# Kernel tuning notes

Measured on AMD Instinct MI355X. Metric: run time of the kernel, lower is better.

## Reference

```python
import jax, jax.numpy as jnp
import numpy as np

L = 2          # n_layer
H = 8          # n_head
DM = 512       # d_model
DFF = 2048     # d_ff
DH = DM // H   # head dim (query_dimensions)
M = DH         # Favor n_dims random features
B, S = 1, 2048
EPS = 1e-6     # causal linear attention eps
LN_EPS = 1e-5  # torch LayerNorm default


def setup_inputs() -> dict:
    key = jax.random.key(0)
    ks = jax.random.split(key, 12)
    sc = 0.02
    d = {}
    d['x'] = jax.random.normal(ks[0], (B, S, DM), dtype=jnp.float32)
    for i, (n, shape) in enumerate([('Wq', (L, DM, DM)), ('Wk', (L, DM, DM)),
                                    ('Wv', (L, DM, DM)), ('Wo', (L, DM, DM)),
                                    ('W1', (L, DM, DFF)), ('W2', (L, DFF, DM))]):
        d[n] = jax.random.normal(ks[i + 1], shape, dtype=jnp.float32) * sc
    d['bq'] = jnp.zeros((L, DM), jnp.float32)
    d['bk'] = jnp.zeros((L, DM), jnp.float32)
    d['bv'] = jnp.zeros((L, DM), jnp.float32)
    d['bo'] = jnp.zeros((L, DM), jnp.float32)
    d['b1'] = jnp.zeros((L, DFF), jnp.float32)
    d['b2'] = jnp.zeros((L, DM), jnp.float32)
    d['g1'] = jnp.ones((L, DM), jnp.float32)
    d['be1'] = jnp.zeros((L, DM), jnp.float32)
    d['g2'] = jnp.ones((L, DM), jnp.float32)
    d['be2'] = jnp.zeros((L, DM), jnp.float32)
    # FAVOR+ random projection matrix per layer: [Dh, M]
    d['omega'] = jax.random.normal(ks[7], (L, DH, M), dtype=jnp.float32)
    return d


def _favor(x, omega):
    # x: [B,S,H,Dh]; softmax_temp = 1/sqrt(Dh) applied as x * sqrt(temp)
    xs = x * (DH ** -0.25)
    nrm = jnp.sum(xs * xs, axis=-1, keepdims=True)       # [B,S,H,1]
    u = jnp.einsum('bshd,dm->bshm', xs, omega)           # [B,S,H,M]
    return jnp.exp(u - 0.5 * nrm) * (M ** -0.5)


def _ln(x, g, b):
    mu = jnp.mean(x, -1, keepdims=True)
    var = jnp.mean((x - mu) ** 2, -1, keepdims=True)
    return (x - mu) * jax.lax.rsqrt(var + LN_EPS) * g + b


def _forward(x, Wq, bq, Wk, bk, Wv, bv, Wo, bo, omega,
             W1, b1, W2, b2, g1, be1, g2, be2):
    out = x
    for l in range(L):
        q = (out @ Wq[l] + bq[l]).reshape(B, S, H, DH)
        k = (out @ Wk[l] + bk[l]).reshape(B, S, H, DH)
        v = (out @ Wv[l] + bv[l]).reshape(B, S, H, DH)
        pq = _favor(q, omega[l])
        pk = _favor(k, omega[l])
        # causal linear attention: running sums of phi(k) v^T and phi(k)
        kv = jnp.cumsum(jnp.einsum('bshm,bshd->bshmd', pk, v), axis=1)  # [B,S,H,M,Dh]
        num = jnp.einsum('bshm,bshmd->bshd', pq, kv)
        den = jnp.einsum('bshm,bshm->bsh', pq, jnp.cumsum(pk, axis=1)) + EPS
        a = (num / den[..., None]).reshape(B, S, DM)
        # post-norm encoder layer (fast-transformers TransformerEncoderLayer)
        out = out + (a @ Wo[l] + bo[l])
        out = _ln(out, g1[l], be1[l])
        y = jax.nn.relu(out @ W1[l] + b1[l]) @ W2[l] + b2[l]
        out = _ln(out + y, g2[l], be2[l])
    return out


def reference(x, Wq, bq, Wk, bk, Wv, bv, Wo, bo, omega,
              W1, b1, W2, b2, g1, be1, g2, be2):
    return _forward(x, Wq, bq, Wk, bk, Wv, bv, Wo, bo, omega,
                    W1, b1, W2, b2, g1, be1, g2, be2)
```

## Files before the change

### kernel.cpp

```cpp
#include <hip/hip_runtime.h>
#include <hip/hip_bf16.h>

#define S_  2048
#define DM_ 512
#define H_  8
#define DH_ 64
#define MF_ 64
#define DFF_ 2048
#define L_  2
#define CT_ 64
#define NC_ (S_ / CT_)
#define EPS_ 1e-6f
#define LN_EPS_ 1e-5f

#define LSW_   3145728
#define W1OFF_ 1048576
#define W2OFF_ 2097152
#define WOOFF_ 786432

typedef unsigned short ushortT;
typedef unsigned int u32;
typedef float f4 __attribute__((ext_vector_type(4)));
typedef short s8 __attribute__((ext_vector_type(8)));
typedef u32 u32x2 __attribute__((ext_vector_type(2)));

__device__ __forceinline__ ushortT f2b(float f) {
  union { float f; unsigned u; } v; v.f = f;
  unsigned r = v.u + 0x7fffu + ((v.u >> 16) & 1u);
  return (ushortT)(r >> 16);
}
__device__ __forceinline__ float bu2f(ushortT h) {
  union { unsigned u; float f; } v; v.u = ((unsigned)h) << 16; return v.f;
}
__device__ __forceinline__ u32 pk2(float a, float b) {
  return (u32)f2b(a) | ((u32)f2b(b) << 16);
}

__global__ __launch_bounds__(256) void tcast_all(
    const float* __restrict__ x,
    const float* __restrict__ Wq, const float* __restrict__ Wk,
    const float* __restrict__ Wv, const float* __restrict__ Wo,
    const float* __restrict__ W1, const float* __restrict__ W2,
    const float* __restrict__ omg,
    float* __restrict__ cur, ushortT* __restrict__ curb,
    ushortT* __restrict__ wb, ushortT* __restrict__ omgTb) {
  const int bid = blockIdx.x;
  const int t = threadIdx.x;
  if (bid >= 6152) {
    const int i = (bid - 6152) * 256 + t;
    float v = x[i];
    cur[i] = v;
    curb[i] = f2b(v);
    return;
  }
  __shared__ ushortT tile[32][33];
  const float* src; ushortT* dst; int K, N, bx, by;
  if (bid < 2048) {
    const int z = bid >> 8, widx = z & 3, lay = z >> 2;
    const float* s4[4] = {Wq, Wk, Wv, Wo};
    src = s4[widx] + (size_t)lay * DM_ * DM_;
    dst = wb + (size_t)lay * LSW_ + (size_t)widx * DM_ * DM_;
    K = DM_; N = DM_; bx = bid & 15; by = (bid >> 4) & 15;
  } else if (bid < 4096) {
    const int r = bid - 2048;
    const int lay = r >> 10;
    src = W1 + (size_t)lay * DM_ * DFF_;
    dst = wb + (size_t)lay * LSW_ + W1OFF_;
    K = DM_; N = DFF_; bx = r & 63; by = (r >> 6) & 15;
  } else if (bid < 6144) {
    const int r = bid - 4096;
    const int lay = r >> 10;
    src = W2 + (size_t)lay * DFF_ * DM_;
    dst = wb + (size_t)lay * LSW_ + W2OFF_;
    K = DFF_; N = DM_; bx = r & 15; by = (r >> 4) & 63;
  } else {
    const int r = bid - 6144;
    const int lay = r >> 2;
    src = omg + (size_t)lay * DH_ * MF_;
    dst = omgTb + (size_t)lay * DH_ * MF_;
    K = DH_; N = MF_; bx = r & 1; by = (r >> 1) & 1;
  }
  const int cc = t & 31, r0 = t >> 5;
  const int n0 = bx * 32, k0 = by * 32;
#pragma unroll
  for (int i = 0; i < 4; ++i) {
    int r = r0 + 8 * i;
    tile[r][cc] = f2b(src[(size_t)(k0 + r) * N + n0 + cc]);
  }
  __syncthreads();
#pragma unroll
  for (int i = 0; i < 4; ++i) {
    int r = r0 + 8 * i;
    dst[(size_t)(n0 + r) * K + k0 + cc] = tile[cc][r];
  }
}

template<bool RELU, bool HAS_RES, bool OUT_BF16>
__global__ __launch_bounds__(256) void mgemm(
    const ushortT* __restrict__ A, const ushortT* __restrict__ Wt,
    const float* __restrict__ bq_, const float* __restrict__ bk_,
    const float* __restrict__ bv_, const float* __restrict__ Res,
    float* __restrict__ Cf, ushortT* __restrict__ Cb, int K, int N) {
  __shared__ ushortT sA[2][2048];
  __shared__ ushortT sB[2][2048];
  const int t = threadIdx.x;
  const int w = t >> 6, l = t & 63;
  const int wm = w >> 1, wn = w & 1;
  const int n0 = blockIdx.x * 64, m0 = blockIdx.y * 64;
  const int z = blockIdx.z;
  const ushortT* Wz = Wt + (size_t)z * K * N;
  const float* bias = (z == 0) ? bq_ : (z == 1 ? bk_ : bv_);

  const int rs = w * 16 + (l >> 2);
  const int qs = (l & 3) ^ ((rs >> 1) & 3);
  const ushortT* gA = A  + (size_t)(m0 + rs) * K + qs * 8;
  const ushortT* gB = Wz + (size_t)(n0 + rs) * K + qs * 8;

  const int Ra = wm * 32 + (l & 15);
  const int Rb = wn * 32 + (l & 15);
  const int qq = l >> 4;
  const int aoff = (Ra * 4 + (qq ^ ((Ra >> 1) & 3))) * 8;
  const int boff = (Rb * 4 + (qq ^ ((Rb >> 1) & 3))) * 8;

  f4 acc[2][2];
#pragma unroll
  for (int i = 0; i < 2; ++i)
#pragma unroll
    for (int j = 0; j < 2; ++j) acc[i][j] = (f4){0.f, 0.f, 0.f, 0.f};

  auto stage = [&](int buf, int ko) {
    __builtin_amdgcn_global_load_lds(
        (const __attribute__((address_space(1))) void*)(gA + ko),
        (__attribute__((address_space(3))) void*)(&sA[buf][w * 512]), 16, 0, 0);
    __builtin_amdgcn_global_load_lds(
        (const __attribute__((address_space(1))) void*)(gB + ko),
        (__attribute__((address_space(3))) void*)(&sB[buf][w * 512]), 16, 0, 0);
  };

  stage(0, 0);
  const int nk = K >> 5;
  for (int ks = 0; ks < nk; ++ks) {
    __syncthreads();
    if (ks + 1 < nk) stage((ks + 1) & 1, (ks + 1) * 32);
    const ushortT* pa = sA[ks & 1];
    const ushortT* pb = sB[ks & 1];
    s8 a0 = *(const s8*)(pa + aoff);
    s8 a1 = *(const s8*)(pa + aoff + 512);
    s8 b0 = *(const s8*)(pb + boff);
    s8 b1 = *(const s8*)(pb + boff + 512);
    acc[0][0] = __builtin_amdgcn_mfma_f32_16x16x32_bf16(a0, b0, acc[0][0], 0, 0, 0);
    acc[0][1] = __builtin_amdgcn_mfma_f32_16x16x32_bf16(a0, b1, acc[0][1], 0, 0, 0);
    acc[1][0] = __builtin_amdgcn_mfma_f32_16x16x32_bf16(a1, b0, acc[1][0], 0, 0, 0);
    acc[1][1] = __builtin_amdgcn_mfma_f32_16x16x32_bf16(a1, b1, acc[1][1], 0, 0, 0);
  }

  const size_t outz = (size_t)z * S_ * N;
  const int colb = n0 + wn * 32 + (l & 15);
  const int rowb = m0 + wm * 32 + ((l >> 4) << 2);
#pragma unroll
  for (int mt = 0; mt < 2; ++mt) {
#pragma unroll
    for (int nt = 0; nt < 2; ++nt) {
      const int c = colb + nt * 16;
      const float bv = bias[c];
#pragma unroll
      for (int r = 0; r < 4; ++r) {
        const int rr = rowb + mt * 16 + r;
        float v = acc[mt][nt][r] + bv;
        if (HAS_RES) v += Res[(size_t)rr * N + c];
        if (RELU) v = fmaxf(v, 0.f);
        if (OUT_BF16) Cb[outz + (size_t)rr * N + c] = f2b(v);
        else          Cf[outz + (size_t)rr * N + c] = v;
      }
    }
  }
}

__global__ __launch_bounds__(256) void mgemm_part(
    const ushortT* __restrict__ A, const ushortT* __restrict__ Wt,
    float* __restrict__ PS, int K, int N, int KS) {
  __shared__ ushortT sA[2][2048];
  __shared__ ushortT sB[2][2048];
  const int t = threadIdx.x;
  const int w = t >> 6, l = t & 63;
  const int wm = w >> 1, wn = w & 1;
  const int n0 = blockIdx.x * 64, m0 = blockIdx.y * 64;
  const int z = blockIdx.z;

  const int rs = w * 16 + (l >> 2);
  const int qs = (l & 3) ^ ((rs >> 1) & 3);
  const ushortT* gA = A  + (size_t)(m0 + rs) * K + z * KS + qs * 8;
  const ushortT* gB = Wt + (size_t)(n0 + rs) * K + z * KS + qs * 8;

  const int Ra = wm * 32 + (l & 15);
  const int Rb = wn * 32 + (l & 15);
  const int qq = l >> 4;
  const int aoff = (Ra * 4 + (qq ^ ((Ra >> 1) & 3))) * 8;
  const int boff = (Rb * 4 + (qq ^ ((Rb >> 1) & 3))) * 8;

  f4 acc[2][2];
#pragma unroll
  for (int i = 0; i < 2; ++i)
#pragma unroll
    for (int j = 0; j < 2; ++j) acc[i][j] = (f4){0.f, 0.f, 0.f, 0.f};

  auto stage = [&](int buf, int ko) {
    __builtin_amdgcn_global_load_lds(
        (const __attribute__((address_space(1))) void*)(gA + ko),
        (__attribute__((address_space(3))) void*)(&sA[buf][w * 512]), 16, 0, 0);
    __builtin_amdgcn_global_load_lds(
        (const __attribute__((address_space(1))) void*)(gB + ko),
        (__attribute__((address_space(3))) void*)(&sB[buf][w * 512]), 16, 0, 0);
  };

  stage(0, 0);
  const int nk = KS >> 5;
  for (int ks = 0; ks < nk; ++ks) {
    __syncthreads();
    if (ks + 1 < nk) stage((ks + 1) & 1, (ks + 1) * 32);
    const ushortT* pa = sA[ks & 1];
    const ushortT* pb = sB[ks & 1];
    s8 a0 = *(const s8*)(pa + aoff);
    s8 a1 = *(const s8*)(pa + aoff + 512);
    s8 b0 = *(const s8*)(pb + boff);
    s8 b1 = *(const s8*)(pb + boff + 512);
    acc[0][0] = __builtin_amdgcn_mfma_f32_16x16x32_bf16(a0, b0, acc[0][0], 0, 0, 0);
    acc[0][1] = __builtin_amdgcn_mfma_f32_16x16x32_bf16(a0, b1, acc[0][1], 0, 0, 0);
    acc[1][0] = __builtin_amdgcn_mfma_f32_16x16x32_bf16(a1, b0, acc[1][0], 0, 0, 0);
    acc[1][1] = __builtin_amdgcn_mfma_f32_16x16x32_bf16(a1, b1, acc[1][1], 0, 0, 0);
  }

  float* out = PS + (size_t)z * S_ * N;
  const int colb = n0 + wn * 32 + (l & 15);
  const int rowb = m0 + wm * 32 + ((l >> 4) << 2);
#pragma unroll
  for (int mt = 0; mt < 2; ++mt) {
#pragma unroll
    for (int nt = 0; nt < 2; ++nt) {
      const int c = colb + nt * 16;
#pragma unroll
      for (int r = 0; r < 4; ++r)
        out[(size_t)(rowb + mt * 16 + r) * N + c] = acc[mt][nt][r];
    }
  }
}

__global__ __launch_bounds__(256) void redln(const float* __restrict__ PS, int nsplit,
                                             const float* __restrict__ bias,
                                             const float* __restrict__ res,
                                             const float* __restrict__ g,
                                             const float* __restrict__ be,
                                             float* __restrict__ outF,
                                             ushortT* __restrict__ outB) {
  const int s = blockIdx.x, t = threadIdx.x;
  float v0 = bias[t] + res[(size_t)s * DM_ + t];
  float v1 = bias[t + 256] + res[(size_t)s * DM_ + 256 + t];
  for (int z = 0; z < nsplit; ++z) {
    const float* p = PS + (size_t)z * S_ * DM_ + (size_t)s * DM_;
    v0 += p[t];
    v1 += p[256 + t];
  }
  float sum = v0 + v1, sq = v0 * v0 + v1 * v1;
  for (int off = 32; off > 0; off >>= 1) {
    sum += __shfl_down(sum, off);
    sq += __shfl_down(sq, off);
  }
  __shared__ float ssum[4], ssq[4];
  __shared__ float smean, srstd;
  const int w = t >> 6;
  if ((t & 63) == 0) { ssum[w] = sum; ssq[w] = sq; }
  __syncthreads();
  if (t == 0) {
    float S1 = ssum[0] + ssum[1] + ssum[2] + ssum[3];
    float S2 = ssq[0] + ssq[1] + ssq[2] + ssq[3];
    float mu = S1 / DM_;
    smean = mu;
    srstd = rsqrtf(S2 / DM_ - mu * mu + LN_EPS_);
  }
  __syncthreads();
  const float mu = smean, rs = srstd;
  float o0 = (v0 - mu) * rs * g[t] + be[t];
  float o1 = (v1 - mu) * rs * g[256 + t] + be[256 + t];
  outF[(size_t)s * DM_ + t] = o0;
  outF[(size_t)s * DM_ + 256 + t] = o1;
  if (outB) {
    outB[(size_t)s * DM_ + t] = f2b(o0);
    outB[(size_t)s * DM_ + 256 + t] = f2b(o1);
  }
}

__global__ __launch_bounds__(256) void favor_cs(const ushortT* __restrict__ qkv,
                                                const ushortT* __restrict__ omgT,
                                                ushortT* __restrict__ PQb,
                                                ushortT* __restrict__ PKb,
                                                float* __restrict__ KVcT,
                                                float* __restrict__ Kc) {
  const int c = blockIdx.x, h = blockIdx.y, t = threadIdx.x;
  const int w = t >> 6, l = t & 63, lr = l & 15, q = l >> 4;
  __shared__ ushortT xq[64 * 72], xk[64 * 72], vT[64 * 72], omT[64 * 72];
  __shared__ ushortT pq[64 * 72], pk[64 * 72], pkT[64 * 72];
  __shared__ float nrm[128];

  const ushortT* qg = qkv + (size_t)(c * CT_) * DM_ + h * DH_;
  const ushortT* kg = qg + (size_t)S_ * DM_;
  const ushortT* vg = kg + (size_t)S_ * DM_;

  for (int i = t; i < 512; i += 256) {
    const int s = i >> 3, seg = i & 7;
    *(s8*)&xq[s * 72 + seg * 8] = *(const s8*)(qg + (size_t)s * DM_ + seg * 8);
    *(s8*)&xk[s * 72 + seg * 8] = *(const s8*)(kg + (size_t)s * DM_ + seg * 8);
    s8 av = *(const s8*)(vg + (size_t)s * DM_ + seg * 8);
#pragma unroll
    for (int j = 0; j < 8; ++j) vT[(seg * 8 + j) * 72 + s] = (ushortT)av[j];
    *(s8*)&omT[s * 72 + seg * 8] = *(const s8*)(omgT + s * 64 + seg * 8);
  }
  __syncthreads();

  if (t < 128) {
    const ushortT* src = (t < 64) ? xq : xk;
    const int s = t & 63;
    float a = 0.f;
#pragma unroll
    for (int seg = 0; seg < 8; ++seg) {
      s8 vv = *(const s8*)(src + s * 72 + seg * 8);
#pragma unroll
      for (int j = 0; j < 8; ++j) {
        float f = bu2f((ushortT)vv[j]);
        a += f * f;
      }
    }
    nrm[t] = a;
  }
  __syncthreads();

  {
    const float gam = 0.35355339059327373f;
    const int s0 = w * 16;
    s8 aq0 = *(const s8*)&xq[(s0 + lr) * 72 + q * 8];
    s8 aq1 = *(const s8*)&xq[(s0 + lr) * 72 + 32 + q * 8];
    s8 ak0 = *(const s8*)&xk[(s0 + lr) * 72 + q * 8];
    s8 ak1 = *(const s8*)&xk[(s0 + lr) * 72 + 32 + q * 8];
#pragma unroll
    for (int mt = 0; mt < 4; ++mt) {
      s8 b0 = *(const s8*)&omT[(mt * 16 + lr) * 72 + q * 8];
      s8 b1 = *(const s8*)&omT[(mt * 16 + lr) * 72 + 32 + q * 8];
      f4 cq = (f4){0.f, 0.f, 0.f, 0.f}, ck = (f4){0.f, 0.f, 0.f, 0.f};
      cq = __builtin_amdgcn_mfma_f32_16x16x32_bf16(aq0, b0, cq, 0, 0, 0);
      cq = __builtin_amdgcn_mfma_f32_16x16x32_bf16(aq1, b1, cq, 0, 0, 0);
      ck = __builtin_amdgcn_mfma_f32_16x16x32_bf16(ak0, b0, ck, 0, 0, 0);
      ck = __builtin_amdgcn_mfma_f32_16x16x32_bf16(ak1, b1, ck, 0, 0, 0);
#pragma unroll
      for (int r = 0; r < 4; ++r) {
        const int sr = s0 + q * 4 + r, mc = mt * 16 + lr;
        float vq = expf(gam * cq[r] - 0.0625f * nrm[sr]) * 0.125f;
        float vk = expf(gam * ck[r] - 0.0625f * nrm[64 + sr]) * 0.125f;
        pq[sr * 72 + mc] = f2b(vq);
        ushortT hk = f2b(vk);
        pk[sr * 72 + mc] = hk;
        pkT[mc * 72 + sr] = hk;
      }
    }
  }
  __syncthreads();

  {
    const int d0 = w * 16;
    s8 a0 = *(const s8*)&vT[(d0 + lr) * 72 + q * 8];
    s8 a1 = *(const s8*)&vT[(d0 + lr) * 72 + 32 + q * 8];
    float* outb = KVcT + (size_t)(h * NC_ + c) * DH_ * MF_;
#pragma unroll
    for (int mt = 0; mt < 4; ++mt) {
      s8 b0 = *(const s8*)&pkT[(mt * 16 + lr) * 72 + q * 8];
      s8 b1 = *(const s8*)&pkT[(mt * 16 + lr) * 72 + 32 + q * 8];
      f4 cc = (f4){0.f, 0.f, 0.f, 0.f};
      cc = __builtin_amdgcn_mfma_f32_16x16x32_bf16(a0, b0, cc, 0, 0, 0);
      cc = __builtin_amdgcn_mfma_f32_16x16x32_bf16(a1, b1, cc, 0, 0, 0);
#pragma unroll
      for (int r = 0; r < 4; ++r)
        outb[(size_t)(d0 + q * 4 + r) * MF_ + mt * 16 + lr] = cc[r];
    }
  }
  if (t < 64) {
    float s = 0.f;
#pragma unroll
    for (int seg = 0; seg < 8; ++seg) {
      s8 vv = *(const s8*)&pkT[t * 72 + seg * 8];
#pragma unroll
      for (int j = 0; j < 8; ++j) s += bu2f((ushortT)vv[j]);
    }
    Kc[(size_t)(h * NC_ + c) * MF_ + t] = s;
  }
  for (int i = t; i < 512; i += 256) {
    const int s = i >> 3, seg = i & 7;
    *(s8*)(PQb + (size_t)(c * CT_ + s) * DM_ + h * MF_ + seg * 8) = *(const s8*)&pq[s * 72 + seg * 8];
    *(s8*)(PKb + (size_t)(c * CT_ + s) * DM_ + h * MF_ + seg * 8) = *(const s8*)&pk[s * 72 + seg * 8];
  }
}

__global__ __launch_bounds__(256) void attn_pfx(const ushortT* __restrict__ PQ,
                                                const ushortT* __restrict__ PK,
                                                const ushortT* __restrict__ V,
                                                const float* __restrict__ KVcT,
                                                const float* __restrict__ Kc,
                                                ushortT* __restrict__ Aout) {
  const int cc = blockIdx.x, h = blockIdx.y, t = threadIdx.x;
  const int w = t >> 6, l = t & 63;
  const int lr = l & 15, q = l >> 4;

  __shared__ ushortT pqs[64 * 72];
  __shared__ ushortT pks[64 * 72];
  __shared__ ushortT vts[64 * 72];
  __shared__ ushortT kvs[64 * 72];
  __shared__ ushortT tms[64 * 72];
  __shared__ float dpart[256];
  __shared__ float den[64];
  __shared__ float kcs[64];

  const int s0j = t >> 3, seg0 = t & 7;
  const int s1j = (t + 256) >> 3, seg1 = t & 7;
  float acc0[8], acc1[8];
#pragma unroll
  for (int j = 0; j < 8; ++j) { acc0[j] = 0.f; acc1[j] = 0.f; }

  const float* kvbase = KVcT + (size_t)(h * NC_) * DH_ * MF_;
  for (int cp = 0; cp < cc; ++cp) {
    const float* kr = kvbase + (size_t)cp * DH_ * MF_;
    f4 a0 = *(const f4*)(kr + s0j * MF_ + seg0 * 8);
    f4 a1 = *(const f4*)(kr + s0j * MF_ + seg0 * 8 + 4);
    f4 b0 = *(const f4*)(kr + s1j * MF_ + seg1 * 8);
    f4 b1 = *(const f4*)(kr + s1j * MF_ + seg1 * 8 + 4);
    acc0[0] += a0.x; acc0[1] += a0.y; acc0[2] += a0.z; acc0[3] += a0.w;
    acc0[4] += a1.x; acc0[5] += a1.y; acc0[6] += a1.z; acc0[7] += a1.w;
    acc1[0] += b0.x; acc1[1] += b0.y; acc1[2] += b0.z; acc1[3] += b0.w;
    acc1[4] += b1.x; acc1[5] += b1.y; acc1[6] += b1.z; acc1[7] += b1.w;
  }
  {
    u32* p0 = (u32*)&kvs[s0j * 72 + seg0 * 8];
    p0[0] = pk2(acc0[0], acc0[1]); p0[1] = pk2(acc0[2], acc0[3]);
    p0[2] = pk2(acc0[4], acc0[5]); p0[3] = pk2(acc0[6], acc0[7]);
    u32* p1 = (u32*)&kvs[s1j * 72 + seg1 * 8];
    p1[0] = pk2(acc1[0], acc1[1]); p1[1] = pk2(acc1[2], acc1[3]);
    p1[2] = pk2(acc1[4], acc1[5]); p1[3] = pk2(acc1[6], acc1[7]);
  }
  if (t < 64) {
    float s = 0.f;
    for (int cp = 0; cp < cc; ++cp) s += Kc[(size_t)(h * NC_ + cp) * MF_ + t];
    kcs[t] = s;
  }

  for (int i = t; i < 512; i += 256) {
    const int s = i >> 3, seg = i & 7;
    *(s8*)&pqs[s * 72 + seg * 8] = *(const s8*)(PQ + (size_t)(cc * CT_ + s) * DM_ + h * MF_ + seg * 8);
    *(s8*)&pks[s * 72 + seg * 8] = *(const s8*)(PK + (size_t)(cc * CT_ + s) * DM_ + h * MF_ + seg * 8);
    s8 av = *(const s8*)(V + (size_t)(cc * CT_ + s) * DM_ + h * DH_ + seg * 8);
#pragma unroll
    for (int j = 0; j < 8; ++j) vts[(seg * 8 + j) * 72 + s] = (ushortT)av[j];
  }
  __syncthreads();

  {
    const int s0 = w * 16;
    s8 a0 = *(const s8*)&pqs[(s0 + lr) * 72 + q * 8];
    s8 a1 = *(const s8*)&pqs[(s0 + lr) * 72 + 32 + q * 8];
#pragma unroll
    for (int tb = 0; tb < 4; ++tb) {
      f4 c = (f4){0.f, 0.f, 0.f, 0.f};
      if (tb <= w) {
        s8 b0 = *(const s8*)&pks[(tb * 16 + lr) * 72 + q * 8];
        s8 b1 = *(const s8*)&pks[(tb * 16 + lr) * 72 + 32 + q * 8];
        c = __builtin_amdgcn_mfma_f32_16x16x32_bf16(a0, b0, c, 0, 0, 0);
        c = __builtin_amdgcn_mfma_f32_16x16x32_bf16(a1, b1, c, 0, 0, 0);
      }
#pragma unroll
      for (int r = 0; r < 4; ++r) {
        float v = c[r];
        if (tb == w && lr > q * 4 + r) v = 0.f;
        tms[(s0 + q * 4 + r) * 72 + tb * 16 + lr] = f2b(v);
      }
    }
  }
  __syncthreads();

  {
    const int s = t >> 2, part = t & 3;
    float dp = 0.f;
    const u32* trow = (const u32*)&tms[s * 72 + part * 16];
#pragma unroll
    for (int j = 0; j < 8; ++j) {
      u32 u = trow[j];
      dp += bu2f((ushortT)(u & 0xffffu)) + bu2f((ushortT)(u >> 16));
    }
    const u32* qrow = (const u32*)&pqs[s * 72 + part * 16];
    const f4* kc4 = (const f4*)(kcs + part * 16);
#pragma unroll
    for (int j = 0; j < 4; ++j) {
      f4 b = kc4[j];
      u32 ua = qrow[2 * j], ub = qrow[2 * j + 1];
      dp += bu2f((ushortT)(ua & 0xffffu)) * b.x + bu2f((ushortT)(ua >> 16)) * b.y +
            bu2f((ushortT)(ub & 0xffffu)) * b.z + bu2f((ushortT)(ub >> 16)) * b.w;
    }
    dpart[t] = dp;
  }
  __syncthreads();
  if (t < 64)
    den[t] = dpart[4 * t] + dpart[4 * t + 1] + dpart[4 * t + 2] + dpart[4 * t + 3] + EPS_;
  __syncthreads();

  {
    const int d0 = w * 16;
    const int drow = d0 + lr;
    s8 akv0 = *(const s8*)&kvs[drow * 72 + q * 8];
    s8 akv1 = *(const s8*)&kvs[drow * 72 + 32 + q * 8];
    s8 av0  = *(const s8*)&vts[drow * 72 + q * 8];
    s8 av1  = *(const s8*)&vts[drow * 72 + 32 + q * 8];
#pragma unroll
    for (int sb = 0; sb < 4; ++sb) {
      const int srow = sb * 16 + lr;
      s8 bq0 = *(const s8*)&pqs[srow * 72 + q * 8];
      s8 bq1 = *(const s8*)&pqs[srow * 72 + 32 + q * 8];
      s8 bt0 = *(const s8*)&tms[srow * 72 + q * 8];
      s8 bt1 = *(const s8*)&tms[srow * 72 + 32 + q * 8];
      f4 c = (f4){0.f, 0.f, 0.f, 0.f};
      c = __builtin_amdgcn_mfma_f32_16x16x32_bf16(akv0, bq0, c, 0, 0, 0);
      c = __builtin_amdgcn_mfma_f32_16x16x32_bf16(akv1, bq1, c, 0, 0, 0);
      c = __builtin_amdgcn_mfma_f32_16x16x32_bf16(av0, bt0, c, 0, 0, 0);
      c = __builtin_amdgcn_mfma_f32_16x16x32_bf16(av1, bt1, c, 0, 0, 0);
      const float inv = 1.f / den[srow];
      u32x2 o;
      o.x = pk2(c[0] * inv, c[1] * inv);
      o.y = pk2(c[2] * inv, c[3] * inv);
      *(u32x2*)(Aout + (size_t)(cc * CT_ + srow) * DM_ + h * DH_ + d0 + q * 4) = o;
    }
  }
}

extern "C" void kernel_launch(void* const* d_in, const int* in_sizes, int n_in,
                              void* d_out, int out_size, void* d_ws, size_t ws_size,
                              hipStream_t stream) {
  const float* x    = (const float*)d_in[0];
  const float* Wq   = (const float*)d_in[1];
  const float* Wk   = (const float*)d_in[2];
  const float* Wv   = (const float*)d_in[3];
  const float* Wo   = (const float*)d_in[4];
  const float* W1   = (const float*)d_in[5];
  const float* W2   = (const float*)d_in[6];
  const float* bq   = (const float*)d_in[7];
  const float* bk   = (const float*)d_in[8];
  const float* bv   = (const float*)d_in[9];
  const float* bo   = (const float*)d_in[10];
  const float* b1   = (const float*)d_in[11];
  const float* b2   = (const float*)d_in[12];
  const float* g1   = (const float*)d_in[13];
  const float* be1  = (const float*)d_in[14];
  const float* g2   = (const float*)d_in[15];
  const float* be2  = (const float*)d_in[16];
  const float* omg  = (const float*)d_in[17];
  float* out = (float*)d_out;

  const size_t MB = 1048576;
  float* f    = (float*)d_ws;
  float* cur  = f;
  float* ln1  = f + 1 * MB;
  float* KVcb = f + 2 * MB;
  float* Kcb  = f + 3 * MB;
  float* PS   = f + 3 * MB + 16384;

  ushortT* u    = (ushortT*)(f + 8 * MB);
  ushortT* curb = u;
  ushortT* qkb  = u + 1 * MB;
  ushortT* pqb  = u + 4 * MB;
  ushortT* pkb  = u + 5 * MB;
  ushortT* qbb  = u + 6 * MB;
  ushortT* ln1b = u + 7 * MB;
  ushortT* ffb  = u + 8 * MB;
  ushortT* wb   = u + 12 * MB;
  ushortT* omgTb = wb + 2 * LSW_;

  tcast_all<<<10248, 256, 0, stream>>>(x, Wq, Wk, Wv, Wo, W1, W2, omg,
                                       cur, curb, wb, omgTb);

  const dim3 gQKV(DM_ / 64, S_ / 64, 3);
  const dim3 gFF1(DFF_ / 64, S_ / 64, 1);
  const dim3 gWo(DM_ / 64, S_ / 64, 2);
  const dim3 gW2(DM_ / 64, S_ / 64, 4);
  const dim3 gAttn(NC_, H_);

  for (int l = 0; l < L_; ++l) {
    const ushortT* wl = wb + (size_t)l * LSW_;
    const size_t bo512 = (size_t)l * DM_;
    const size_t boFF = (size_t)l * DFF_;

    mgemm<false, false, true><<<gQKV, 256, 0, stream>>>(
        curb, wl, bq + bo512, bk + bo512, bv + bo512, nullptr, nullptr, qkb, DM_, DM_);

    favor_cs<<<gAttn, 256, 0, stream>>>(qkb, omgTb + (size_t)l * DH_ * MF_,
                                        pqb, pkb, KVcb, Kcb);
    attn_pfx<<<gAttn, 256, 0, stream>>>(pqb, pkb, qkb + 2 * (size_t)S_ * DM_,
                                        KVcb, Kcb, qbb);

    mgemm_part<<<gWo, 256, 0, stream>>>(qbb, wl + WOOFF_, PS, DM_, DM_, 256);
    redln<<<S_, 256, 0, stream>>>(PS, 2, bo + bo512, cur, g1 + bo512, be1 + bo512, ln1, ln1b);

    mgemm<true, false, true><<<gFF1, 256, 0, stream>>>(
        ln1b, wl + W1OFF_, b1 + boFF, nullptr, nullptr, nullptr, nullptr, ffb, DM_, DFF_);

    mgemm_part<<<gW2, 256, 0, stream>>>(ffb, wl + W2OFF_, PS, DFF_, DM_, 512);
    const bool last = (l == L_ - 1);
    redln<<<S_, 256, 0, stream>>>(PS, 4, b2 + bo512, ln1, g2 + bo512, be2 + bo512,
                                  last ? out : cur, last ? nullptr : curb);
  }
}
```

Before: 264.8 us.

## Fuse QKV GEMM, FAVOR features and causal prefix attention into one kernel

Replaces the separate QKV GEMM, favor_cs and attn_pfx launches with a single attn_mega kernel per layer. Each block computes its 64-row by head slice of Q, K and V directly into shared memory, builds the feature maps, publishes its chunk KV/K sums, then spin-waits on per-chunk release/acquire flags before doing the prefix attention. This removes two launches and the global round-trips for qkv, PQ and PK. In exchange it relies on cross-block flag synchronisation, which assumes all earlier chunks' blocks make progress (256 blocks should fit co-resident). It uses only 256 blocks for the QKV GEMM, giving less parallelism than the previous 768-block grid.

```diff
diff --git a/kernel.cpp b/kernel.cpp
--- a/kernel.cpp
+++ b/kernel.cpp
@@ -43,9 +43,15 @@
     const float* __restrict__ W1, const float* __restrict__ W2,
     const float* __restrict__ omg,
     float* __restrict__ cur, ushortT* __restrict__ curb,
-    ushortT* __restrict__ wb, ushortT* __restrict__ omgTb) {
+    ushortT* __restrict__ wb, ushortT* __restrict__ omgTb,
+    u32* __restrict__ flags) {
   const int bid = blockIdx.x;
   const int t = threadIdx.x;
+  if (bid == 10248) {
+    flags[t] = 0u;
+    flags[t + 256] = 0u;
+    return;
+  }
   if (bid >= 6152) {
     const int i = (bid - 6152) * 256 + t;
     float v = x[i];
@@ -98,8 +104,7 @@
 template<bool RELU, bool HAS_RES, bool OUT_BF16>
 __global__ __launch_bounds__(256) void mgemm(
     const ushortT* __restrict__ A, const ushortT* __restrict__ Wt,
-    const float* __restrict__ bq_, const float* __restrict__ bk_,
-    const float* __restrict__ bv_, const float* __restrict__ Res,
+    const float* __restrict__ bias, const float* __restrict__ Res,
     float* __restrict__ Cf, ushortT* __restrict__ Cb, int K, int N) {
   __shared__ ushortT sA[2][2048];
   __shared__ ushortT sB[2][2048];
@@ -107,14 +112,11 @@
   const int w = t >> 6, l = t & 63;
   const int wm = w >> 1, wn = w & 1;
   const int n0 = blockIdx.x * 64, m0 = blockIdx.y * 64;
-  const int z = blockIdx.z;
-  const ushortT* Wz = Wt + (size_t)z * K * N;
-  const float* bias = (z == 0) ? bq_ : (z == 1 ? bk_ : bv_);
 
   const int rs = w * 16 + (l >> 2);
   const int qs = (l & 3) ^ ((rs >> 1) & 3);
   const ushortT* gA = A  + (size_t)(m0 + rs) * K + qs * 8;
-  const ushortT* gB = Wz + (size_t)(n0 + rs) * K + qs * 8;
+  const ushortT* gB = Wt + (size_t)(n0 + rs) * K + qs * 8;
 
   const int Ra = wm * 32 + (l & 15);
   const int Rb = wn * 32 + (l & 15);
@@ -154,7 +156,6 @@
     acc[1][1] = __builtin_amdgcn_mfma_f32_16x16x32_bf16(a1, b1, acc[1][1], 0, 0, 0);
   }
 
-  const size_t outz = (size_t)z * S_ * N;
   const int colb = n0 + wn * 32 + (l & 15);
   const int rowb = m0 + wm * 32 + ((l >> 4) << 2);
 #pragma unroll
@@ -169,8 +170,8 @@
         float v = acc[mt][nt][r] + bv;
         if (HAS_RES) v += Res[(size_t)rr * N + c];
         if (RELU) v = fmaxf(v, 0.f);
-        if (OUT_BF16) Cb[outz + (size_t)rr * N + c] = f2b(v);
-        else          Cf[outz + (size_t)rr * N + c] = v;
+        if (OUT_BF16) Cb[(size_t)rr * N + c] = f2b(v);
+        else          Cf[(size_t)rr * N + c] = v;
       }
     }
   }
@@ -289,30 +290,104 @@
   }
 }
 
-__global__ __launch_bounds__(256) void favor_cs(const ushortT* __restrict__ qkv,
-                                                const ushortT* __restrict__ omgT,
-                                                ushortT* __restrict__ PQb,
-                                                ushortT* __restrict__ PKb,
-                                                float* __restrict__ KVcT,
-                                                float* __restrict__ Kc) {
-  const int c = blockIdx.x, h = blockIdx.y, t = threadIdx.x;
+__global__ __launch_bounds__(256) void attn_mega(
+    const ushortT* __restrict__ curb, const ushortT* __restrict__ wl,
+    const float* __restrict__ bq, const float* __restrict__ bk,
+    const float* __restrict__ bv, const ushortT* __restrict__ omgT,
+    float* __restrict__ KVc, float* __restrict__ Kc,
+    u32* __restrict__ flags, ushortT* __restrict__ Aout) {
+  const int cc = blockIdx.x, h = blockIdx.y, t = threadIdx.x;
   const int w = t >> 6, l = t & 63, lr = l & 15, q = l >> 4;
-  __shared__ ushortT xq[64 * 72], xk[64 * 72], vT[64 * 72], omT[64 * 72];
-  __shared__ ushortT pq[64 * 72], pk[64 * 72], pkT[64 * 72];
-  __shared__ float nrm[128];
-
-  const ushortT* qg = qkv + (size_t)(c * CT_) * DM_ + h * DH_;
-  const ushortT* kg = qg + (size_t)S_ * DM_;
-  const ushortT* vg = kg + (size_t)S_ * DM_;
-
-  for (int i = t; i < 512; i += 256) {
-    const int s = i >> 3, seg = i & 7;
-    *(s8*)&xq[s * 72 + seg * 8] = *(const s8*)(qg + (size_t)s * DM_ + seg * 8);
-    *(s8*)&xk[s * 72 + seg * 8] = *(const s8*)(kg + (size_t)s * DM_ + seg * 8);
-    s8 av = *(const s8*)(vg + (size_t)s * DM_ + seg * 8);
-#pragma unroll
-    for (int j = 0; j < 8; ++j) vT[(seg * 8 + j) * 72 + s] = (ushortT)av[j];
-    *(s8*)&omT[s * 72 + seg * 8] = *(const s8*)(omgT + s * 64 + seg * 8);
+  const int wm = w >> 1, wn = w & 1;
+
+  __shared__ char smem[65536];
+  ushortT* sA  = (ushortT*)smem;
+  ushortT* sB  = sA + 4096;
+  ushortT* xq  = (ushortT*)smem;
+  ushortT* xk  = xq + 4608;
+  ushortT* vT  = xk + 4608;
+  ushortT* omT = vT + 4608;
+  ushortT* pq  = omT + 4608;
+  ushortT* pk  = pq + 4608;
+  ushortT* pkT = pk + 4608;
+  float* nrm = (float*)(smem + 64512);
+  float* den = (float*)(smem + 65024);
+  float* kcs = (float*)(smem + 65280);
+  ushortT* kvs = xq;
+  ushortT* tms = xk;
+
+  const int m0 = cc * 64, n0 = h * 64;
+  const int rs = w * 16 + (l >> 2);
+  const int qs2 = (l & 3) ^ ((rs >> 1) & 3);
+  const ushortT* gA = curb + (size_t)(m0 + rs) * DM_ + qs2 * 8;
+  const ushortT* gB = wl + (size_t)(n0 + rs) * DM_ + qs2 * 8;
+
+  const int Ra = wm * 32 + lr;
+  const int Rb = wn * 32 + lr;
+  const int aoff = (Ra * 4 + (q ^ ((Ra >> 1) & 3))) * 8;
+  const int boff = (Rb * 4 + (q ^ ((Rb >> 1) & 3))) * 8;
+
+  f4 acc[3][2][2];
+#pragma unroll
+  for (int z = 0; z < 3; ++z)
+#pragma unroll
+    for (int i = 0; i < 2; ++i)
+#pragma unroll
+      for (int j = 0; j < 2; ++j) acc[z][i][j] = (f4){0.f, 0.f, 0.f, 0.f};
+
+  auto stage = [&](int buf, int ko) {
+    __builtin_amdgcn_global_load_lds(
+        (const __attribute__((address_space(1))) void*)(gA + ko),
+        (__attribute__((address_space(3))) void*)(sA + buf * 2048 + w * 512), 16, 0, 0);
+#pragma unroll
+    for (int z = 0; z < 3; ++z)
+      __builtin_amdgcn_global_load_lds(
+          (const __attribute__((address_space(1))) void*)(gB + (size_t)z * DM_ * DM_ + ko),
+          (__attribute__((address_space(3))) void*)(sB + buf * 6144 + z * 2048 + w * 512), 16, 0, 0);
+  };
+
+  stage(0, 0);
+  for (int ks = 0; ks < 16; ++ks) {
+    __syncthreads();
+    if (ks + 1 < 16) stage((ks + 1) & 1, (ks + 1) * 32);
+    const ushortT* pa = sA + (ks & 1) * 2048;
+    s8 a0 = *(const s8*)(pa + aoff);
+    s8 a1 = *(const s8*)(pa + aoff + 512);
+#pragma unroll
+    for (int z = 0; z < 3; ++z) {
+      const ushortT* pb = sB + (ks & 1) * 6144 + z * 2048;
+      s8 b0 = *(const s8*)(pb + boff);
+      s8 b1 = *(const s8*)(pb + boff + 512);
+      acc[z][0][0] = __builtin_amdgcn_mfma_f32_16x16x32_bf16(a0, b0, acc[z][0][0], 0, 0, 0);
+      acc[z][0][1] = __builtin_amdgcn_mfma_f32_16x16x32_bf16(a0, b1, acc[z][0][1], 0, 0, 0);
+      acc[z][1][0] = __builtin_amdgcn_mfma_f32_16x16x32_bf16(a1, b0, acc[z][1][0], 0, 0, 0);
+      acc[z][1][1] = __builtin_amdgcn_mfma_f32_16x16x32_bf16(a1, b1, acc[z][1][1], 0, 0, 0);
+    }
+  }
+  __syncthreads();
+
+  {
+    const int colL = wn * 32 + lr;
+    const int rowL = wm * 32 + q * 4;
+#pragma unroll
+    for (int mt = 0; mt < 2; ++mt) {
+#pragma unroll
+      for (int nt = 0; nt < 2; ++nt) {
+        const int col = colL + nt * 16;
+        const float bqv = bq[n0 + col], bkv = bk[n0 + col], bvv = bv[n0 + col];
+#pragma unroll
+        for (int r = 0; r < 4; ++r) {
+          const int row = rowL + mt * 16 + r;
+          xq[row * 72 + col] = f2b(acc[0][mt][nt][r] + bqv);
+          xk[row * 72 + col] = f2b(acc[1][mt][nt][r] + bkv);
+          vT[col * 72 + row] = f2b(acc[2][mt][nt][r] + bvv);
+        }
+      }
+    }
+    for (int i = t; i < 512; i += 256) {
+      const int s = i >> 3, seg = i & 7;
+      *(s8*)&omT[s * 72 + seg * 8] = *(const s8*)(omgT + s * 64 + seg * 8);
+    }
   }
   __syncthreads();
 
@@ -367,17 +442,17 @@
     const int d0 = w * 16;
     s8 a0 = *(const s8*)&vT[(d0 + lr) * 72 + q * 8];
     s8 a1 = *(const s8*)&vT[(d0 + lr) * 72 + 32 + q * 8];
-    float* outb = KVcT + (size_t)(h * NC_ + c) * DH_ * MF_;
+    float* outb = KVc + (size_t)(h * NC_ + cc) * DH_ * MF_;
 #pragma unroll
     for (int mt = 0; mt < 4; ++mt) {
       s8 b0 = *(const s8*)&pkT[(mt * 16 + lr) * 72 + q * 8];
       s8 b1 = *(const s8*)&pkT[(mt * 16 + lr) * 72 + 32 + q * 8];
-      f4 cc = (f4){0.f, 0.f, 0.f, 0.f};
-      cc = __builtin_amdgcn_mfma_f32_16x16x32_bf16(a0, b0, cc, 0, 0, 0);
-      cc = __builtin_amdgcn_mfma_f32_16x16x32_bf16(a1, b1, cc, 0, 0, 0);
+      f4 cs = (f4){0.f, 0.f, 0.f, 0.f};
+      cs = __builtin_amdgcn_mfma_f32_16x16x32_bf16(a0, b0, cs, 0, 0, 0);
+      cs = __builtin_amdgcn_mfma_f32_16x16x32_bf16(a1, b1, cs, 0, 0, 0);
 #pragma unroll
       for (int r = 0; r < 4; ++r)
-        outb[(size_t)(d0 + q * 4 + r) * MF_ + mt * 16 + lr] = cc[r];
+        outb[(size_t)(d0 + q * 4 + r) * MF_ + mt * 16 + lr] = cs[r];
     }
   }
   if (t < 64) {
@@ -388,92 +463,68 @@
 #pragma unroll
       for (int j = 0; j < 8; ++j) s += bu2f((ushortT)vv[j]);
     }
-    Kc[(size_t)(h * NC_ + c) * MF_ + t] = s;
-  }
-  for (int i = t; i < 512; i += 256) {
-    const int s = i >> 3, seg = i & 7;
-    *(s8*)(PQb + (size_t)(c * CT_ + s) * DM_ + h * MF_ + seg * 8) = *(const s8*)&pq[s * 72 + seg * 8];
-    *(s8*)(PKb + (size_t)(c * CT_ + s) * DM_ + h * MF_ + seg * 8) = *(const s8*)&pk[s * 72 + seg * 8];
-  }
-}
-
-__global__ __launch_bounds__(256) void attn_pfx(const ushortT* __restrict__ PQ,
-                                                const ushortT* __restrict__ PK,
-                                                const ushortT* __restrict__ V,
-                                                const float* __restrict__ KVcT,
-                                                const float* __restrict__ Kc,
-                                                ushortT* __restrict__ Aout) {
-  const int cc = blockIdx.x, h = blockIdx.y, t = threadIdx.x;
-  const int w = t >> 6, l = t & 63;
-  const int lr = l & 15, q = l >> 4;
-
-  __shared__ ushortT pqs[64 * 72];
-  __shared__ ushortT pks[64 * 72];
-  __shared__ ushortT vts[64 * 72];
-  __shared__ ushortT kvs[64 * 72];
-  __shared__ ushortT tms[64 * 72];
-  __shared__ float dpart[256];
-  __shared__ float den[64];
-  __shared__ float kcs[64];
-
-  const int s0j = t >> 3, seg0 = t & 7;
-  const int s1j = (t + 256) >> 3, seg1 = t & 7;
-  float acc0[8], acc1[8];
-#pragma unroll
-  for (int j = 0; j < 8; ++j) { acc0[j] = 0.f; acc1[j] = 0.f; }
-
-  const float* kvbase = KVcT + (size_t)(h * NC_) * DH_ * MF_;
-  for (int cp = 0; cp < cc; ++cp) {
-    const float* kr = kvbase + (size_t)cp * DH_ * MF_;
-    f4 a0 = *(const f4*)(kr + s0j * MF_ + seg0 * 8);
-    f4 a1 = *(const f4*)(kr + s0j * MF_ + seg0 * 8 + 4);
-    f4 b0 = *(const f4*)(kr + s1j * MF_ + seg1 * 8);
-    f4 b1 = *(const f4*)(kr + s1j * MF_ + seg1 * 8 + 4);
-    acc0[0] += a0.x; acc0[1] += a0.y; acc0[2] += a0.z; acc0[3] += a0.w;
-    acc0[4] += a1.x; acc0[5] += a1.y; acc0[6] += a1.z; acc0[7] += a1.w;
-    acc1[0] += b0.x; acc1[1] += b0.y; acc1[2] += b0.z; acc1[3] += b0.w;
-    acc1[4] += b1.x; acc1[5] += b1.y; acc1[6] += b1.z; acc1[7] += b1.w;
-  }
+    Kc[(size_t)(h * NC_ + cc) * MF_ + t] = s;
+  }
+  __threadfence();
+  __syncthreads();
+  if (t == 0)
+    __hip_atomic_store(&flags[h * NC_ + cc], 1u, __ATOMIC_RELEASE, __HIP_MEMORY_SCOPE_AGENT);
+
+  for (int cp = t; cp < cc; cp += 256)
+    while (__hip_atomic_load(&flags[h * NC_ + cp], __ATOMIC_ACQUIRE,
+                             __HIP_MEMORY_SCOPE_AGENT) == 0u)
+      __builtin_amdgcn_s_sleep(1);
+  __syncthreads();
+  __threadfence();
+
   {
+    const int s0j = t >> 3, seg0 = t & 7;
+    const int s1j = (t + 256) >> 3;
+    float a0v[8], a1v[8];
+#pragma unroll
+    for (int j = 0; j < 8; ++j) { a0v[j] = 0.f; a1v[j] = 0.f; }
+    const float* kvbase = KVc + (size_t)(h * NC_) * DH_ * MF_;
+    for (int cp = 0; cp < cc; ++cp) {
+      const float* kr = kvbase + (size_t)cp * DH_ * MF_;
+      f4 x0 = *(const f4*)(kr + s0j * MF_ + seg0 * 8);
+      f4 x1 = *(const f4*)(kr + s0j * MF_ + seg0 * 8 + 4);
+      f4 y0 = *(const f4*)(kr + s1j * MF_ + seg0 * 8);
+      f4 y1 = *(const f4*)(kr + s1j * MF_ + seg0 * 8 + 4);
+      a0v[0] += x0.x; a0v[1] += x0.y; a0v[2] += x0.z; a0v[3] += x0.w;
+      a0v[4] += x1.x; a0v[5] += x1.y; a0v[6] += x1.z; a0v[7] += x1.w;
+      a1v[0] += y0.x; a1v[1] += y0.y; a1v[2] += y0.z; a1v[3] += y0.w;
+      a1v[4] += y1.x; a1v[5] += y1.y; a1v[6] += y1.z; a1v[7] += y1.w;
+    }
     u32* p0 = (u32*)&kvs[s0j * 72 + seg0 * 8];
-    p0[0] = pk2(acc0[0], acc0[1]); p0[1] = pk2(acc0[2], acc0[3]);
-    p0[2] = pk2(acc0[4], acc0[5]); p0[3] = pk2(acc0[6], acc0[7]);
-    u32* p1 = (u32*)&kvs[s1j * 72 + seg1 * 8];
-    p1[0] = pk2(acc1[0], acc1[1]); p1[1] = pk2(acc1[2], acc1[3]);
-    p1[2] = pk2(acc1[4], acc1[5]); p1[3] = pk2(acc1[6], acc1[7]);
+    p0[0] = pk2(a0v[0], a0v[1]); p0[1] = pk2(a0v[2], a0v[3]);
+    p0[2] = pk2(a0v[4], a0v[5]); p0[3] = pk2(a0v[6], a0v[7]);
+    u32* p1 = (u32*)&kvs[s1j * 72 + seg0 * 8];
+    p1[0] = pk2(a1v[0], a1v[1]); p1[1] = pk2(a1v[2], a1v[3]);
+    p1[2] = pk2(a1v[4], a1v[5]); p1[3] = pk2(a1v[6], a1v[7]);
   }
   if (t < 64) {
     float s = 0.f;
     for (int cp = 0; cp < cc; ++cp) s += Kc[(size_t)(h * NC_ + cp) * MF_ + t];
     kcs[t] = s;
   }
-
-  for (int i = t; i < 512; i += 256) {
-    const int s = i >> 3, seg = i & 7;
-    *(s8*)&pqs[s * 72 + seg * 8] = *(const s8*)(PQ + (size_t)(cc * CT_ + s) * DM_ + h * MF_ + seg * 8);
-    *(s8*)&pks[s * 72 + seg * 8] = *(const s8*)(PK + (size_t)(cc * CT_ + s) * DM_ + h * MF_ + seg * 8);
-    s8 av = *(const s8*)(V + (size_t)(cc * CT_ + s) * DM_ + h * DH_ + seg * 8);
-#pragma unroll
-    for (int j = 0; j < 8; ++j) vts[(seg * 8 + j) * 72 + s] = (ushortT)av[j];
-  }
   __syncthreads();
 
   {
     const int s0 = w * 16;
-    s8 a0 = *(const s8*)&pqs[(s0 + lr) * 72 + q * 8];
-    s8 a1 = *(const s8*)&pqs[(s0 + lr) * 72 + 32 + q * 8];
+    s8 a0 = *(const s8*)&pq[(s0 + lr) * 72 + q * 8];
+    s8 a1 = *(const s8*)&pq[(s0 + lr) * 72 + 32 + q * 8];
 #pragma unroll
     for (int tb = 0; tb < 4; ++tb) {
-      f4 c = (f4){0.f, 0.f, 0.f, 0.f};
+      f4 cs = (f4){0.f, 0.f, 0.f, 0.f};
       if (tb <= w) {
-        s8 b0 = *(const s8*)&pks[(tb * 16 + lr) * 72 + q * 8];
-        s8 b1 = *(const s8*)&pks[(tb * 16 + lr) * 72 + 32 + q * 8];
-        c = __builtin_amdgcn_mfma_f32_16x16x32_bf16(a0, b0, c, 0, 0, 0);
-        c = __builtin_amdgcn_mfma_f32_16x16x32_bf16(a1, b1, c, 0, 0, 0);
+        s8 b0 = *(const s8*)&pk[(tb * 16 + lr) * 72 + q * 8];
+        s8 b1 = *(const s8*)&pk[(tb * 16 + lr) * 72 + 32 + q * 8];
+        cs = __builtin_amdgcn_mfma_f32_16x16x32_bf16(a0, b0, cs, 0, 0, 0);
+        cs = __builtin_amdgcn_mfma_f32_16x16x32_bf16(a1, b1, cs, 0, 0, 0);
       }
 #pragma unroll
       for (int r = 0; r < 4; ++r) {
-        float v = c[r];
+        float v = cs[r];
         if (tb == w && lr > q * 4 + r) v = 0.f;
         tms[(s0 + q * 4 + r) * 72 + tb * 16 + lr] = f2b(v);
       }
@@ -490,7 +541,7 @@
       u32 u = trow[j];
       dp += bu2f((ushortT)(u & 0xffffu)) + bu2f((ushortT)(u >> 16));
     }
-    const u32* qrow = (const u32*)&pqs[s * 72 + part * 16];
+    const u32* qrow = (const u32*)&pq[s * 72 + part * 16];
     const f4* kc4 = (const f4*)(kcs + part * 16);
 #pragma unroll
     for (int j = 0; j < 4; ++j) {
@@ -499,11 +550,10 @@
       dp += bu2f((ushortT)(ua & 0xffffu)) * b.x + bu2f((ushortT)(ua >> 16)) * b.y +
             bu2f((ushortT)(ub & 0xffffu)) * b.z + bu2f((ushortT)(ub >> 16)) * b.w;
     }
-    dpart[t] = dp;
-  }
-  __syncthreads();
-  if (t < 64)
-    den[t] = dpart[4 * t] + dpart[4 * t + 1] + dpart[4 * t + 2] + dpart[4 * t + 3] + EPS_;
+    dp += __shfl_down(dp, 2);
+    dp += __shfl_down(dp, 1);
+    if (part == 0) den[s] = dp + EPS_;
+  }
   __syncthreads();
 
   {
@@ -511,24 +561,24 @@
     const int drow = d0 + lr;
     s8 akv0 = *(const s8*)&kvs[drow * 72 + q * 8];
     s8 akv1 = *(const s8*)&kvs[drow * 72 + 32 + q * 8];
-    s8 av0  = *(const s8*)&vts[drow * 72 + q * 8];
-    s8 av1  = *(const s8*)&vts[drow * 72 + 32 + q * 8];
+    s8 av0  = *(const s8*)&vT[drow * 72 + q * 8];
+    s8 av1  = *(const s8*)&vT[drow * 72 + 32 + q * 8];
 #pragma unroll
     for (int sb = 0; sb < 4; ++sb) {
       const int srow = sb * 16 + lr;
-      s8 bq0 = *(const s8*)&pqs[srow * 72 + q * 8];
-      s8 bq1 = *(const s8*)&pqs[srow * 72 + 32 + q * 8];
+      s8 bq0 = *(const s8*)&pq[srow * 72 + q * 8];
+      s8 bq1 = *(const s8*)&pq[srow * 72 + 32 + q * 8];
       s8 bt0 = *(const s8*)&tms[srow * 72 + q * 8];
       s8 bt1 = *(const s8*)&tms[srow * 72 + 32 + q * 8];
-      f4 c = (f4){0.f, 0.f, 0.f, 0.f};
-      c = __builtin_amdgcn_mfma_f32_16x16x32_bf16(akv0, bq0, c, 0, 0, 0);
-      c = __builtin_amdgcn_mfma_f32_16x16x32_bf16(akv1, bq1, c, 0, 0, 0);
-      c = __builtin_amdgcn_mfma_f32_16x16x32_bf16(av0, bt0, c, 0, 0, 0);
-      c = __builtin_amdgcn_mfma_f32_16x16x32_bf16(av1, bt1, c, 0, 0, 0);
+      f4 cs = (f4){0.f, 0.f, 0.f, 0.f};
+      cs = __builtin_amdgcn_mfma_f32_16x16x32_bf16(akv0, bq0, cs, 0, 0, 0);
+      cs = __builtin_amdgcn_mfma_f32_16x16x32_bf16(akv1, bq1, cs, 0, 0, 0);
+      cs = __builtin_amdgcn_mfma_f32_16x16x32_bf16(av0, bt0, cs, 0, 0, 0);
+      cs = __builtin_amdgcn_mfma_f32_16x16x32_bf16(av1, bt1, cs, 0, 0, 0);
       const float inv = 1.f / den[srow];
       u32x2 o;
-      o.x = pk2(c[0] * inv, c[1] * inv);
-      o.y = pk2(c[2] * inv, c[3] * inv);
+      o.x = pk2(cs[0] * inv, cs[1] * inv);
+      o.y = pk2(cs[2] * inv, cs[3] * inv);
       *(u32x2*)(Aout + (size_t)(cc * CT_ + srow) * DM_ + h * DH_ + d0 + q * 4) = o;
     }
   }
@@ -558,28 +608,25 @@
   float* out = (float*)d_out;
 
   const size_t MB = 1048576;
-  float* f    = (float*)d_ws;
-  float* cur  = f;
-  float* ln1  = f + 1 * MB;
-  float* KVcb = f + 2 * MB;
-  float* Kcb  = f + 3 * MB;
-  float* PS   = f + 3 * MB + 16384;
+  float* f     = (float*)d_ws;
+  float* cur   = f;
+  float* ln1   = f + 1 * MB;
+  float* KVcb  = f + 2 * MB;
+  float* Kcb   = f + 3 * MB;
+  u32*   flagb = (u32*)(f + 3 * MB + 16384);
+  float* PS    = f + 3 * MB + 32768;
 
   ushortT* u    = (ushortT*)(f + 8 * MB);
   ushortT* curb = u;
-  ushortT* qkb  = u + 1 * MB;
-  ushortT* pqb  = u + 4 * MB;
-  ushortT* pkb  = u + 5 * MB;
-  ushortT* qbb  = u + 6 * MB;
-  ushortT* ln1b = u + 7 * MB;
-  ushortT* ffb  = u + 8 * MB;
-  ushortT* wb   = u + 12 * MB;
+  ushortT* qbb  = u + 1 * MB;
+  ushortT* ln1b = u + 2 * MB;
+  ushortT* ffb  = u + 3 * MB;
+  ushortT* wb   = u + 7 * MB;
   ushortT* omgTb = wb + 2 * LSW_;
 
-  tcast_all<<<10248, 256, 0, stream>>>(x, Wq, Wk, Wv, Wo, W1, W2, omg,
-                                       cur, curb, wb, omgTb);
-
-  const dim3 gQKV(DM_ / 64, S_ / 64, 3);
+  tcast_all<<<10249, 256, 0, stream>>>(x, Wq, Wk, Wv, Wo, W1, W2, omg,
+                                       cur, curb, wb, omgTb, flagb);
+
   const dim3 gFF1(DFF_ / 64, S_ / 64, 1);
   const dim3 gWo(DM_ / 64, S_ / 64, 2);
   const dim3 gW2(DM_ / 64, S_ / 64, 4);
@@ -590,19 +637,16 @@
     const size_t bo512 = (size_t)l * DM_;
     const size_t boFF = (size_t)l * DFF_;
 
-    mgemm<false, false, true><<<gQKV, 256, 0, stream>>>(
-        curb, wl, bq + bo512, bk + bo512, bv + bo512, nullptr, nullptr, qkb, DM_, DM_);
-
-    favor_cs<<<gAttn, 256, 0, stream>>>(qkb, omgTb + (size_t)l * DH_ * MF_,
-                                        pqb, pkb, KVcb, Kcb);
-    attn_pfx<<<gAttn, 256, 0, stream>>>(pqb, pkb, qkb + 2 * (size_t)S_ * DM_,
-                                        KVcb, Kcb, qbb);
+    attn_mega<<<gAttn, 256, 0, stream>>>(
+        curb, wl, bq + bo512, bk + bo512, bv + bo512,
+        omgTb + (size_t)l * DH_ * MF_, KVcb, Kcb,
+        flagb + (size_t)l * H_ * NC_, qbb);
 
     mgemm_part<<<gWo, 256, 0, stream>>>(qbb, wl + WOOFF_, PS, DM_, DM_, 256);
     redln<<<S_, 256, 0, stream>>>(PS, 2, bo + bo512, cur, g1 + bo512, be1 + bo512, ln1, ln1b);
 
     mgemm<true, false, true><<<gFF1, 256, 0, stream>>>(
-        ln1b, wl + W1OFF_, b1 + boFF, nullptr, nullptr, nullptr, nullptr, ffb, DM_, DFF_);
+        ln1b, wl + W1OFF_, b1 + boFF, nullptr, nullptr, ffb, DM_, DFF_);
 
     mgemm_part<<<gW2, 256, 0, stream>>>(ffb, wl + W2OFF_, PS, DFF_, DM_, 512);
     const bool last = (l == L_ - 1);
```

Result: slower. 348.2 us (+31.5%).
